# Kernel tuning notes

Measured on AMD Instinct MI355X. Metric: run time of the kernel, lower is better.

The kernel has to match this reference:

```python
import jax, jax.numpy as jnp
import numpy as np
import math

B, S, STATE, H, D = 4, 2048, 1024, 16, 64
N_ROT = 32  # int(0.5*64), even
ROPE_BASE = 10000.0


def setup_inputs() -> dict:
    key = jax.random.key(0)
    ks = jax.random.split(key, 8)
    q_src = jax.random.normal(ks[0], (B, S, STATE), jnp.float32)
    k_src = jax.random.normal(ks[1], (B, S, STATE), jnp.float32)
    v_src = jax.random.normal(ks[2], (B, S, STATE), jnp.float32)
    # causal position mask: True = masked (torch masked_fill semantics)
    position_mask = jnp.triu(jnp.ones((S, S), jnp.bool_), k=1)
    sd = 0.02
    Wq = jax.random.normal(ks[3], (H * D, STATE), jnp.float32) * sd
    Wk = jax.random.normal(ks[4], (H * D, STATE), jnp.float32) * sd
    Wv = jax.random.normal(ks[5], (H * D, STATE), jnp.float32) * sd
    Wo = jax.random.normal(ks[6], (STATE, H * D), jnp.float32) * sd
    return {"q_src": q_src, "k_src": k_src, "v_src": v_src,
            "position_mask": position_mask,
            "Wq": Wq, "Wk": Wk, "Wv": Wv, "Wo": Wo}


def _rotate_half(x):
    x1, x2 = jnp.split(x, 2, axis=-1)
    return jnp.concatenate([-x2, x1], axis=-1)


def _rope(q, k, offset):
    # q,k: [B,H,S,N_ROT]; positions: k at arange(Sk), q at offset+arange(Sq)
    inv_freq = 1.0 / (ROPE_BASE ** (jnp.arange(0, N_ROT, 2, dtype=jnp.float32) / N_ROT))
    def sincos(pos):
        freqs = pos[:, None] * inv_freq[None, :]          # [S, N_ROT/2]
        emb = jnp.concatenate([freqs, freqs], axis=-1)    # [S, N_ROT]
        return jnp.sin(emb), jnp.cos(emb)
    sk, ck = sincos(jnp.arange(k.shape[-2], dtype=jnp.float32))
    sq, cq = sincos(offset + jnp.arange(q.shape[-2], dtype=jnp.float32))
    q = q * cq + _rotate_half(q) * sq
    k = k * ck + _rotate_half(k) * sk
    return q, k


def reference(q_src, k_src, v_src, position_mask, Wq, Wk, Wv, Wo):
    qk_scale = (1.0 / math.sqrt(D)) ** 0.5  # sqrt of 1/sqrt(D), applied to q and k
    def heads(x):  # [B,S,H*D] -> [B,H,S,D]
        return x.reshape(B, S, H, D).transpose(0, 2, 1, 3)
    q = heads((q_src @ Wq.T) * qk_scale)
    k = heads((k_src @ Wk.T) * qk_scale)
    v = heads(v_src @ Wv.T)
    # inline RoPE on first N_ROT dims (pos_offset = 0, no kv cache)
    rq, rk = _rope(q[..., :N_ROT], k[..., :N_ROT], 0.0)
    q = jnp.concatenate([rq, q[..., N_ROT:]], axis=-1)
    k = jnp.concatenate([rk, k[..., N_ROT:]], axis=-1)
    att = jnp.einsum('bhqd,bhkd->bhqk', q, k)
    att = jnp.where(position_mask[None, None], -jnp.inf, att)
    att = jax.nn.softmax(att, axis=-1)
    out = jnp.einsum('bhqk,bhkd->bhqd', att, v)
    out = out.transpose(0, 2, 1, 3).reshape(B, S, H * D)
    return out @ Wo.T
```

## Files before the change

### kernel.cpp

```cpp
#include <hip/hip_runtime.h>

typedef unsigned short u16;
typedef unsigned int u32;
typedef short short8 __attribute__((ext_vector_type(8)));
typedef float f32x4 __attribute__((ext_vector_type(4)));
typedef float f32x16 __attribute__((ext_vector_type(16)));

#define NB 4
#define NS 2048
#define NSTATE 1024
#define NH 16
#define ND 64
#define NM (NB*NS)

#if __has_builtin(__builtin_amdgcn_exp2f)
#define EXP2(x) __builtin_amdgcn_exp2f(x)
#else
#define EXP2(x) __expf((x) * 0.6931471805599453f)
#endif

__device__ __forceinline__ u16 f2bf(float f){
  union { float fv; unsigned uv; } x; x.fv = f;
  unsigned r = x.uv + 0x7fffu + ((x.uv >> 16) & 1u);
  return (u16)(r >> 16);
}

__device__ __forceinline__ u32 cvtpk(float lo, float hi){
  u32 r;
  asm("v_cvt_pk_bf16_f32 %0, %1, %2" : "=v"(r) : "v"(lo), "v"(hi));
  return r;
}

__device__ __forceinline__ f32x4 mfma16x16(short8 a, short8 b, f32x4 c){
  return __builtin_amdgcn_mfma_f32_16x16x32_bf16(a, b, c, 0, 0, 0);
}

__device__ __forceinline__ f32x16 mfma32(short8 a, short8 b, f32x16 c){
  return __builtin_amdgcn_mfma_f32_32x32x16_bf16(a, b, c, 0, 0, 0);
}

__device__ __forceinline__ void gld_lds16(const u16* g, u16* l){
  __builtin_amdgcn_global_load_lds((const __attribute__((address_space(1))) void*)g,
                                   (__attribute__((address_space(3))) void*)l, 16, 0, 0);
}

__global__ __launch_bounds__(256)
void cvt_all(const float* __restrict__ q, const float* __restrict__ k, const float* __restrict__ v,
             const float* __restrict__ wq, const float* __restrict__ wk,
             const float* __restrict__ wv, const float* __restrict__ wo,
             u16* oq, u16* ok, u16* ov, u16* owq, u16* owk, u16* owv, u16* owo){
  const int XN4 = (NB*NS*NSTATE)/4;
  const int WN4 = (NSTATE*NSTATE)/4;
  int gid = blockIdx.x * 256 + threadIdx.x;
  const float* src; u16* dst; int idx;
  if (gid < XN4)          { src = q; dst = oq; idx = gid; }
  else if (gid < 2*XN4)   { src = k; dst = ok; idx = gid - XN4; }
  else if (gid < 3*XN4)   { src = v; dst = ov; idx = gid - 2*XN4; }
  else {
    int g = gid - 3*XN4;
    int wsel = g >> 18;
    idx = g & (WN4 - 1);
    src = (wsel==0)?wq:(wsel==1)?wk:(wsel==2)?wv:wo;
    dst = (wsel==0)?owq:(wsel==1)?owk:(wsel==2)?owv:owo;
  }
  float4 val = ((const float4*)src)[idx];
  ushort4 r;
  r.x = f2bf(val.x); r.y = f2bf(val.y); r.z = f2bf(val.z); r.w = f2bf(val.w);
  ((ushort4*)dst)[idx] = r;
}

__global__ __launch_bounds__(256)
void gemm_qkv(const u16* __restrict__ xq, const u16* __restrict__ xk,
              const u16* __restrict__ xv, const u16* __restrict__ Wcat,
              u16* __restrict__ Qh, u16* __restrict__ Kk, u16* __restrict__ Vt){
  __shared__ __align__(16) u16 As[128*64];
  __shared__ __align__(16) u16 Bs[128*64];
  const int gblk = blockIdx.x;
  const int wid = (gblk & 7) * 192 + (gblk >> 3);
  const int bx = wid % 24, by = wid / 24;
  const int sel = bx >> 3;
  const u16* A = (sel==0) ? xq : (sel==1) ? xk : xv;
  const int tid = threadIdx.x;
  const int lane = tid & 63, w = tid >> 6;
  const int wr = w >> 1, wc = w & 1;
  const int l15 = lane & 15, lhi = lane >> 4;
  const int brow = by * 128;
  const int bcol = bx * 128;
  const int K = NSTATE;
  f32x4 acc[4][4] = {};

  for (int kt = 0; kt < K; kt += 64){
    #pragma unroll
    for (int it = 0; it < 4; ++it){
      int flat = it*4096 + tid*16;
      int row = flat >> 7, colb = flat & 127;
      gld_lds16(A + (size_t)(brow+row)*K + kt + (colb>>1), As + (flat>>1));
    }
    #pragma unroll
    for (int it = 0; it < 4; ++it){
      int flat = it*4096 + tid*16;
      int row = flat >> 7, colb = flat & 127;
      gld_lds16(Wcat + (size_t)(bcol+row)*K + kt + (colb>>1), Bs + (flat>>1));
    }
    __syncthreads();
    #pragma unroll
    for (int ks = 0; ks < 2; ++ks){
      short8 av[4], bv[4];
      #pragma unroll
      for (int i = 0; i < 4; ++i)
        av[i] = *(const short8*)&As[(wr*64 + i*16 + l15)*64 + ks*32 + lhi*8];
      #pragma unroll
      for (int j = 0; j < 4; ++j)
        bv[j] = *(const short8*)&Bs[(wc*64 + j*16 + l15)*64 + ks*32 + lhi*8];
      #pragma unroll
      for (int i = 0; i < 4; ++i)
        #pragma unroll
        for (int j = 0; j < 4; ++j)
          acc[i][j] = mfma16x16(av[i], bv[j], acc[i][j]);
    }
    __syncthreads();
  }

  const int col0 = bcol + wc*64;
  if (sel == 2){
    const int head = (col0 & 1023) >> 6;
    #pragma unroll
    for (int i = 0; i < 4; ++i){
      int m0 = brow + wr*64 + i*16 + lhi*4;
      int b = m0 >> 11, s0 = m0 & (NS-1);
      u16* obase = Vt + ((size_t)((b*NH + head)*ND))*NS + s0;
      #pragma unroll
      for (int j = 0; j < 4; ++j){
        int d = j*16 + l15;
        uint2 pk;
        pk.x = cvtpk(acc[i][j][0], acc[i][j][1]);
        pk.y = cvtpk(acc[i][j][2], acc[i][j][3]);
        *(uint2*)(obase + (size_t)d*NS) = pk;
      }
    }
  } else {
    u16* out = sel ? Kk : Qh;
    const float qk_scale = 0.4246609f;
    const int head = (col0 & 1023) >> 6;
    const float invf = __powf(10000.0f, -(float)l15 * (1.0f/16.0f));
    #pragma unroll
    for (int i = 0; i < 4; ++i){
      #pragma unroll
      for (int reg = 0; reg < 4; ++reg){
        int m = brow + wr*64 + i*16 + lhi*4 + reg;
        int b = m >> 11, s = m & (NS-1);
        float sn, cs;
        __sincosf((float)s * invf, &sn, &cs);
        float x0 = acc[i][0][reg]*qk_scale;
        float x1 = acc[i][1][reg]*qk_scale;
        u16* orow = out + ((size_t)(b*NH + head)*NS + s)*ND;
        orow[ 0 + l15] = f2bf(x0*cs - x1*sn);
        orow[16 + l15] = f2bf(x1*cs + x0*sn);
        orow[32 + l15] = f2bf(acc[i][2][reg]*qk_scale);
        orow[48 + l15] = f2bf(acc[i][3][reg]*qk_scale);
      }
    }
  }
}

__global__ __launch_bounds__(256)
void gemm_wo(const u16* __restrict__ A, const u16* __restrict__ Bt, float* __restrict__ out){
  __shared__ __align__(16) u16 As[128*64];
  __shared__ __align__(16) u16 Bs[128*64];
  const int gblk = blockIdx.x;
  const int wid = (gblk & 7) * 64 + (gblk >> 3);
  const int bx = wid & 7, by = wid >> 3;
  const int tid = threadIdx.x;
  const int lane = tid & 63, w = tid >> 6;
  const int wr = w >> 1, wc = w & 1;
  const int l15 = lane & 15, lhi = lane >> 4;
  const int brow = by * 128;
  const int bcol = bx * 128;
  const int K = NSTATE;
  f32x4 acc[4][4] = {};

  for (int kt = 0; kt < K; kt += 64){
    #pragma unroll
    for (int it = 0; it < 4; ++it){
      int flat = it*4096 + tid*16;
      int row = flat >> 7, colb = flat & 127;
      gld_lds16(A + (size_t)(brow+row)*K + kt + (colb>>1), As + (flat>>1));
    }
    #pragma unroll
    for (int it = 0; it < 4; ++it){
      int flat = it*4096 + tid*16;
      int row = flat >> 7, colb = flat & 127;
      gld_lds16(Bt + (size_t)(bcol+row)*K + kt + (colb>>1), Bs + (flat>>1));
    }
    __syncthreads();
    #pragma unroll
    for (int ks = 0; ks < 2; ++ks){
      short8 av[4], bv[4];
      #pragma unroll
      for (int i = 0; i < 4; ++i)
        av[i] = *(const short8*)&As[(wr*64 + i*16 + l15)*64 + ks*32 + lhi*8];
      #pragma unroll
      for (int j = 0; j < 4; ++j)
        bv[j] = *(const short8*)&Bs[(wc*64 + j*16 + l15)*64 + ks*32 + lhi*8];
      #pragma unroll
      for (int i = 0; i < 4; ++i)
        #pragma unroll
        for (int j = 0; j < 4; ++j)
          acc[i][j] = mfma16x16(av[i], bv[j], acc[i][j]);
    }
    __syncthreads();
  }
  #pragma unroll
  for (int i = 0; i < 4; ++i)
    #pragma unroll
    for (int reg = 0; reg < 4; ++reg){
      int m = brow + wr*64 + i*16 + lhi*4 + reg;
      float* orow = out + (size_t)m*NSTATE + bcol + wc*64;
      #pragma unroll
      for (int j = 0; j < 4; ++j)
        orow[j*16 + l15] = acc[i][j][reg];
    }
}

__global__ __launch_bounds__(256)
void flash_attn(const u16* __restrict__ Q, const u16* __restrict__ Kh,
                const u16* __restrict__ Vt, u16* __restrict__ O){
  __shared__ __align__(16) u16 Kbuf[2][64*64];
  __shared__ __align__(16) u16 Vbuf[2][64*64];
  const int gblk = blockIdx.x;
  const int xcd = gblk & 7, gr = gblk >> 3;
  const int bh  = xcd*8 + (gr & 7);
  const int g   = 15 - (gr >> 3);
  const int tid = threadIdx.x;
  const int w = tid >> 6, lane = tid & 63;
  const int l31 = lane & 31, hi = lane >> 5;
  const u16* Qb = Q  + (size_t)bh*NS*ND;
  const u16* Kb = Kh + (size_t)bh*NS*ND;
  const u16* Vb = Vt + (size_t)bh*ND*NS;
  const int b = bh >> 4, h = bh & 15;
  const int qw = g*128 + w*32;
  const int kend_w   = qw + 32;
  const int kend_blk = g*128 + 128;

  short8 qf[4];
  #pragma unroll
  for (int dd = 0; dd < 4; ++dd)
    qf[dd] = *(const short8*)&Qb[(size_t)(qw + l31)*ND + dd*16 + hi*8];

  f32x16 oacc[2] = {};
  float mrun = 8.0f, lrun = 0.f;

  int cur = 0;
  #pragma unroll
  for (int i = 0; i < 2; ++i){
    int ch = i*256 + tid;
    int row = ch >> 3, cc = ch & 7;
    int scc = cc ^ (row & 7);
    gld_lds16(Kb + (size_t)row*ND + scc*8, &Kbuf[cur][ch*8]);
    gld_lds16(Vb + (size_t)row*NS + scc*8, &Vbuf[cur][ch*8]);
  }
  __syncthreads();

  #pragma unroll 1
  for (int kv0 = 0; kv0 < kend_blk; kv0 += 64){
    if (kv0 + 64 < kend_blk){
      #pragma unroll
      for (int i = 0; i < 2; ++i){
        int ch = i*256 + tid;
        int row = ch >> 3, cc = ch & 7;
        int scc = cc ^ (row & 7);
        gld_lds16(Kb + (size_t)(kv0 + 64 + row)*ND + scc*8, &Kbuf[cur^1][ch*8]);
        gld_lds16(Vb + (size_t)row*NS + kv0 + 64 + scc*8, &Vbuf[cur^1][ch*8]);
      }
    }
    if (kv0 < kend_w){
      const char* kb = (const char*)&Kbuf[cur][0];
      const char* vb = (const char*)&Vbuf[cur][0];
      short8 kf[8];
      #pragma unroll
      for (int kh2 = 0; kh2 < 2; ++kh2)
        #pragma unroll
        for (int dd = 0; dd < 4; ++dd){
          int srow = kh2*32 + l31;
          int off = (srow*128 + dd*32 + hi*16) ^ ((srow & 7) << 4);
          kf[kh2*4+dd] = *(const short8*)(kb + off);
        }
      f32x16 st0 = {}, st1 = {};
      __builtin_amdgcn_s_setprio(1);
      #pragma unroll
      for (int dd = 0; dd < 4; ++dd) st0 = mfma32(kf[dd],   qf[dd], st0);
      #pragma unroll
      for (int dd = 0; dd < 4; ++dd) st1 = mfma32(kf[4+dd], qf[dd], st1);
      __builtin_amdgcn_s_setprio(0);
      if (kv0 + 63 > qw){
        int q = qw + l31;
        #pragma unroll
        for (int r2 = 0; r2 < 16; ++r2){
          int k0 = kv0 + (r2 & 3) + 8*(r2 >> 2) + 4*hi;
          if (k0      > q) st0[r2] = -3.0e30f;
          if (k0 + 32 > q) st1[r2] = -3.0e30f;
        }
      }
      float m0 = fmaxf(fmaxf(st0[0], st0[1]), fmaxf(st0[2], st0[3]));
      float m1 = fmaxf(fmaxf(st0[4], st0[5]), fmaxf(st0[6], st0[7]));
      float m2 = fmaxf(fmaxf(st0[8], st0[9]), fmaxf(st0[10], st0[11]));
      float m3 = fmaxf(fmaxf(st0[12], st0[13]), fmaxf(st0[14], st0[15]));
      float m4 = fmaxf(fmaxf(st1[0], st1[1]), fmaxf(st1[2], st1[3]));
      float m5 = fmaxf(fmaxf(st1[4], st1[5]), fmaxf(st1[6], st1[7]));
      float m6 = fmaxf(fmaxf(st1[8], st1[9]), fmaxf(st1[10], st1[11]));
      float m7 = fmaxf(fmaxf(st1[12], st1[13]), fmaxf(st1[14], st1[15]));
      float pm = fmaxf(fmaxf(fmaxf(m0, m1), fmaxf(m2, m3)),
                       fmaxf(fmaxf(m4, m5), fmaxf(m6, m7)));
      pm = fmaxf(pm, __shfl_xor(pm, 32));
      #pragma unroll
      for (int r2 = 0; r2 < 16; ++r2){
        st0[r2] = EXP2(st0[r2] - mrun);
        st1[r2] = EXP2(st1[r2] - mrun);
      }
      float s0 = 0.f, s1 = 0.f, s2 = 0.f, s3 = 0.f;
      #pragma unroll
      for (int r2 = 0; r2 < 16; r2 += 4){
        s0 += st0[r2+0] + st1[r2+0];
        s1 += st0[r2+1] + st1[r2+1];
        s2 += st0[r2+2] + st1[r2+2];
        s3 += st0[r2+3] + st1[r2+3];
      }
      float rs = (s0 + s1) + (s2 + s3);
      rs += __shfl_xor(rs, 32);
      if (__any(pm > mrun)){
        float mn = fmaxf(mrun, pm);
        float a  = EXP2(mrun - mn);
        mrun = mn;
        lrun = (lrun + rs) * a;
        #pragma unroll
        for (int r2 = 0; r2 < 16; ++r2){
          st0[r2] *= a; st1[r2] *= a;
          oacc[0][r2] *= a; oacc[1][r2] *= a;
        }
      } else {
        lrun += rs;
      }
      short8 paf[4];
      #pragma unroll
      for (int sl = 0; sl < 4; ++sl){
        const f32x16& S = (sl < 2) ? st0 : st1;
        const int base = (sl & 1) * 8;
        u32 a0 = cvtpk(S[base+0], S[base+1]);
        u32 b0 = cvtpk(S[base+4], S[base+5]);
        asm("v_permlane32_swap_b32 %0, %1" : "+v"(a0), "+v"(b0));
        u32 a1 = cvtpk(S[base+2], S[base+3]);
        u32 b1 = cvtpk(S[base+6], S[base+7]);
        asm("v_permlane32_swap_b32 %0, %1" : "+v"(a1), "+v"(b1));
        union { u32 u[4]; short8 v; } pk_;
        pk_.u[0] = a0; pk_.u[1] = a1; pk_.u[2] = b0; pk_.u[3] = b1;
        paf[sl] = pk_.v;
      }
      #pragma unroll
      for (int dh = 0; dh < 2; ++dh){
        short8 vv[4];
        #pragma unroll
        for (int sl = 0; sl < 4; ++sl){
          int drow = dh*32 + l31;
          int off = (drow*128 + sl*32 + hi*16) ^ ((drow & 7) << 4);
          vv[sl] = *(const short8*)(vb + off);
        }
        __builtin_amdgcn_s_setprio(1);
        #pragma unroll
        for (int sl = 0; sl < 4; ++sl)
          oacc[dh] = mfma32(vv[sl], paf[sl], oacc[dh]);
        __builtin_amdgcn_s_setprio(0);
      }
    }
    __syncthreads();
    cur ^= 1;
  }

  float inv = 1.0f / lrun;
  u16* orow = O + ((size_t)(b*NS + qw + l31))*NSTATE + h*ND;
  #pragma unroll
  for (int dh = 0; dh < 2; ++dh)
    #pragma unroll
    for (int rq = 0; rq < 4; ++rq){
      uint2 pk;
      pk.x = cvtpk(oacc[dh][rq*4+0]*inv, oacc[dh][rq*4+1]*inv);
      pk.y = cvtpk(oacc[dh][rq*4+2]*inv, oacc[dh][rq*4+3]*inv);
      *(uint2*)(orow + dh*32 + rq*8 + hi*4) = pk;
    }
}

extern "C" void kernel_launch(void* const* d_in, const int* in_sizes, int n_in,
                              void* d_out, int out_size, void* d_ws, size_t ws_size,
                              hipStream_t stream){
  const float* q_src = (const float*)d_in[0];
  const float* k_src = (const float*)d_in[1];
  const float* v_src = (const float*)d_in[2];
  const float* Wq = (const float*)d_in[4];
  const float* Wk = (const float*)d_in[5];
  const float* Wv = (const float*)d_in[6];
  const float* Wo = (const float*)d_in[7];

  char* ws = (char*)d_ws;
  const size_t MB = 1u << 20;
  if (ws_size < 104*MB) return;

  u16* xq   = (u16*)(ws +  0*MB);
  u16* xk   = (u16*)(ws + 16*MB);
  u16* xv   = (u16*)(ws + 32*MB);
  u16* wq16 = (u16*)(ws + 48*MB);
  u16* wk16 = (u16*)(ws + 50*MB);
  u16* wv16 = (u16*)(ws + 52*MB);
  u16* wo16 = (u16*)(ws + 54*MB);
  u16* Qh   = (u16*)(ws + 56*MB);
  u16* Kk   = (u16*)(ws + 72*MB);
  u16* Vt   = (u16*)(ws + 88*MB);
  u16* Oat  = xk;

  cvt_all<<<dim3(28672), dim3(256), 0, stream>>>(q_src, k_src, v_src, Wq, Wk, Wv, Wo,
                                                 xq, xk, xv, wq16, wk16, wv16, wo16);
  gemm_qkv<<<dim3(1536), dim3(256), 0, stream>>>(xq, xk, xv, wq16, Qh, Kk, Vt);
  flash_attn<<<dim3(1024), dim3(256), 0, stream>>>(Qh, Kk, Vt, Oat);
  gemm_wo<<<dim3(512), dim3(256), 0, stream>>>(Oat, wo16, (float*)d_out);
}
```

Before: 216.0 us.

## Restructure QKV GEMM into 256x256 tiles with 4-stage async LDS pipeline

Rewrites the QKV projection GEMM to use 256x256 output tiles with 512 threads, a 4-deep ring of K=32 LDS buffers filled via global_load_lds, and XOR-swizzled LDS layout to avoid bank conflicts. Explicit vmcnt waits and single barriers per step let loads for future tiles overlap MFMA work, replacing the old load-sync-compute-sync loop. It also raises MFMA priority and computes the RoPE frequency with exp2. Larger tiles increase reuse but raise register pressure (128 accumulators per lane) and reduce the block count to 384.

```diff
diff --git a/kernel.cpp b/kernel.cpp
--- a/kernel.cpp
+++ b/kernel.cpp
@@ -43,6 +43,8 @@
   __builtin_amdgcn_global_load_lds((const __attribute__((address_space(1))) void*)g,
                                    (__attribute__((address_space(3))) void*)l, 16, 0, 0);
 }
+
+#define FENCE() __builtin_amdgcn_sched_barrier(0)
 
 __global__ __launch_bounds__(256)
 void cvt_all(const float* __restrict__ q, const float* __restrict__ k, const float* __restrict__ v,
@@ -69,64 +71,99 @@
   ((ushort4*)dst)[idx] = r;
 }
 
-__global__ __launch_bounds__(256)
+__global__ __launch_bounds__(512)
 void gemm_qkv(const u16* __restrict__ xq, const u16* __restrict__ xk,
               const u16* __restrict__ xv, const u16* __restrict__ Wcat,
               u16* __restrict__ Qh, u16* __restrict__ Kk, u16* __restrict__ Vt){
-  __shared__ __align__(16) u16 As[128*64];
-  __shared__ __align__(16) u16 Bs[128*64];
+  __shared__ __align__(16) u16 Ab[4][256*32];
+  __shared__ __align__(16) u16 Bb[4][256*32];
   const int gblk = blockIdx.x;
-  const int wid = (gblk & 7) * 192 + (gblk >> 3);
-  const int bx = wid % 24, by = wid / 24;
-  const int sel = bx >> 3;
+  const int wid = (gblk & 7) * 48 + (gblk >> 3);
+  const int bx = wid % 12, by = wid / 12;
+  const int sel = bx >> 2;
   const u16* A = (sel==0) ? xq : (sel==1) ? xk : xv;
   const int tid = threadIdx.x;
   const int lane = tid & 63, w = tid >> 6;
-  const int wr = w >> 1, wc = w & 1;
+  const int wr = w >> 2, wc = w & 3;
   const int l15 = lane & 15, lhi = lane >> 4;
-  const int brow = by * 128;
-  const int bcol = bx * 128;
+  const int brow = by*256, bcol = bx*256;
   const int K = NSTATE;
-  f32x4 acc[4][4] = {};
-
-  for (int kt = 0; kt < K; kt += 64){
-    #pragma unroll
-    for (int it = 0; it < 4; ++it){
-      int flat = it*4096 + tid*16;
-      int row = flat >> 7, colb = flat & 127;
-      gld_lds16(A + (size_t)(brow+row)*K + kt + (colb>>1), As + (flat>>1));
-    }
-    #pragma unroll
-    for (int it = 0; it < 4; ++it){
-      int flat = it*4096 + tid*16;
-      int row = flat >> 7, colb = flat & 127;
-      gld_lds16(Wcat + (size_t)(bcol+row)*K + kt + (colb>>1), Bs + (flat>>1));
-    }
-    __syncthreads();
-    #pragma unroll
-    for (int ks = 0; ks < 2; ++ks){
-      short8 av[4], bv[4];
-      #pragma unroll
-      for (int i = 0; i < 4; ++i)
-        av[i] = *(const short8*)&As[(wr*64 + i*16 + l15)*64 + ks*32 + lhi*8];
-      #pragma unroll
-      for (int j = 0; j < 4; ++j)
-        bv[j] = *(const short8*)&Bs[(wc*64 + j*16 + l15)*64 + ks*32 + lhi*8];
-      #pragma unroll
-      for (int i = 0; i < 4; ++i)
-        #pragma unroll
-        for (int j = 0; j < 4; ++j)
-          acc[i][j] = mfma16x16(av[i], bv[j], acc[i][j]);
-    }
-    __syncthreads();
-  }
+
+  f32x4 acc[8][4] = {};
+
+  auto stage = [&](int t, int b){
+    const int kt = t*32;
+    #pragma unroll
+    for (int i2 = 0; i2 < 2; ++i2){
+      int ch = i2*512 + tid;
+      int row = ch >> 2, cc = ch & 3;
+      int scc = cc ^ (row & 3);
+      gld_lds16(A + (size_t)(brow+row)*K + kt + scc*8, &Ab[b][ch*8]);
+    }
+    #pragma unroll
+    for (int i2 = 0; i2 < 2; ++i2){
+      int ch = i2*512 + tid;
+      int row = ch >> 2, cc = ch & 3;
+      int scc = cc ^ (row & 3);
+      gld_lds16(Wcat + (size_t)(bcol+row)*K + kt + scc*8, &Bb[b][ch*8]);
+    }
+  };
+
+  auto compute = [&](int b){
+    const u16* Ax = &Ab[b][0];
+    const u16* Bx = &Bb[b][0];
+    #pragma unroll
+    for (int ih = 0; ih < 2; ++ih){
+      short8 av[4];
+      #pragma unroll
+      for (int i = 0; i < 4; ++i){
+        int row = wr*128 + ih*64 + i*16 + l15;
+        av[i] = *(const short8*)&Ax[row*32 + ((lhi ^ (row&3))*8)];
+      }
+      #pragma unroll
+      for (int jh = 0; jh < 2; ++jh){
+        short8 bv[2];
+        #pragma unroll
+        for (int j = 0; j < 2; ++j){
+          int row = wc*64 + jh*32 + j*16 + l15;
+          bv[j] = *(const short8*)&Bx[row*32 + ((lhi ^ (row&3))*8)];
+        }
+        __builtin_amdgcn_s_setprio(1);
+        #pragma unroll
+        for (int i = 0; i < 4; ++i)
+          #pragma unroll
+          for (int j = 0; j < 2; ++j)
+            acc[ih*4+i][jh*2+j] = mfma16x16(av[i], bv[j], acc[ih*4+i][jh*2+j]);
+        __builtin_amdgcn_s_setprio(0);
+      }
+    }
+  };
+
+  stage(0, 0); stage(1, 1); stage(2, 2);
+
+  #pragma unroll 1
+  for (int t = 0; t < 29; ++t){
+    asm volatile("s_waitcnt vmcnt(8)" ::: "memory");
+    FENCE(); __builtin_amdgcn_s_barrier(); FENCE();
+    stage(t+3, (t+3)&3);
+    compute(t&3);
+  }
+  asm volatile("s_waitcnt vmcnt(8)" ::: "memory");
+  FENCE(); __builtin_amdgcn_s_barrier(); FENCE();
+  compute(29&3);
+  asm volatile("s_waitcnt vmcnt(4)" ::: "memory");
+  FENCE(); __builtin_amdgcn_s_barrier(); FENCE();
+  compute(30&3);
+  asm volatile("s_waitcnt vmcnt(0)" ::: "memory");
+  FENCE(); __builtin_amdgcn_s_barrier(); FENCE();
+  compute(31&3);
 
   const int col0 = bcol + wc*64;
   if (sel == 2){
     const int head = (col0 & 1023) >> 6;
     #pragma unroll
-    for (int i = 0; i < 4; ++i){
-      int m0 = brow + wr*64 + i*16 + lhi*4;
+    for (int i = 0; i < 8; ++i){
+      int m0 = brow + wr*128 + i*16 + lhi*4;
       int b = m0 >> 11, s0 = m0 & (NS-1);
       u16* obase = Vt + ((size_t)((b*NH + head)*ND))*NS + s0;
       #pragma unroll
@@ -142,12 +179,12 @@
     u16* out = sel ? Kk : Qh;
     const float qk_scale = 0.4246609f;
     const int head = (col0 & 1023) >> 6;
-    const float invf = __powf(10000.0f, -(float)l15 * (1.0f/16.0f));
-    #pragma unroll
-    for (int i = 0; i < 4; ++i){
+    const float invf = EXP2(-0.83048202f * (float)l15);
+    #pragma unroll
+    for (int i = 0; i < 8; ++i){
       #pragma unroll
       for (int reg = 0; reg < 4; ++reg){
-        int m = brow + wr*64 + i*16 + lhi*4 + reg;
+        int m = brow + wr*128 + i*16 + lhi*4 + reg;
         int b = m >> 11, s = m & (NS-1);
         float sn, cs;
         __sincosf((float)s * invf, &sn, &cs);
@@ -417,7 +454,7 @@
 
   cvt_all<<<dim3(28672), dim3(256), 0, stream>>>(q_src, k_src, v_src, Wq, Wk, Wv, Wo,
                                                  xq, xk, xv, wq16, wk16, wv16, wo16);
-  gemm_qkv<<<dim3(1536), dim3(256), 0, stream>>>(xq, xk, xv, wq16, Qh, Kk, Vt);
+  gemm_qkv<<<dim3(384), dim3(512), 0, stream>>>(xq, xk, xv, wq16, Qh, Kk, Vt);
   flash_attn<<<dim3(1024), dim3(256), 0, stream>>>(Qh, Kk, Vt, Oat);
   gemm_wo<<<dim3(512), dim3(256), 0, stream>>>(Oat, wo16, (float*)d_out);
 }
```

Result: slower. 224.0 us (+3.7%).
